# Kernel optimization log

Hardware: AMD Instinct MI355X
Metric: run time of the kernel (lower is better)

Reference implementation:

```python
import jax, jax.numpy as jnp
import numpy as np

HID = 2048
HEADS = 16
HD = HID // HEADS  # 128


def setup_inputs() -> dict:
    key = jax.random.key(0)
    ks = jax.random.split(key, 9)
    s = 0.02
    return {
        "hidden_state": jax.random.normal(ks[0], (2, 2048, HID), dtype=jnp.float32),
        "Wq": jax.random.normal(ks[1], (HID, HID), dtype=jnp.float32) * s,
        "bq": jnp.zeros((HID,), dtype=jnp.float32),
        "Wk": jax.random.normal(ks[2], (HID, HD), dtype=jnp.float32) * s,
        "bk": jnp.zeros((HD,), dtype=jnp.float32),
        "Wv": jax.random.normal(ks[3], (HID, HD), dtype=jnp.float32) * s,
        "bv": jnp.zeros((HD,), dtype=jnp.float32),
        "Wo": jax.random.normal(ks[4], (HID, HID), dtype=jnp.float32) * s,
        "bo": jnp.zeros((HID,), dtype=jnp.float32),
    }


def reference(hidden_state, Wq, bq, Wk, bk, Wv, bv, Wo, bo):
    bs, seq, _ = hidden_state.shape
    # Q: [b, s, H, hd] -> per-head; K,V: single shared head [b, s, hd]
    q = (hidden_state @ Wq + bq).reshape(bs, seq, HEADS, HD)
    k = hidden_state @ Wk + bk  # [b, s, hd]
    v = hidden_state @ Wv + bv  # [b, s, hd]
    scale = 1.0 / jnp.sqrt(jnp.float32(HD))
    # scores: [b, h, s_q, s_k] against shared K head
    scores = jnp.einsum("bqhd,bkd->bhqk", q, k) * scale
    attn = jax.nn.softmax(scores, axis=-1)
    out = jnp.einsum("bhqk,bkd->bqhd", attn, v)  # [b, s, h, hd]
    out = out.reshape(bs, seq, HID)
    return out @ Wo + bo
```

## Files before the change

### kernel.cpp

```cpp
#include <hip/hip_runtime.h>
#include <math.h>

#define HIDN 2048
#define NHEADS 16
#define HDIM 128
#define SEQ 2048
#define NB 2

typedef __bf16 bf16x8 __attribute__((ext_vector_type(8)));
typedef float f32x4 __attribute__((ext_vector_type(4)));

__device__ __forceinline__ unsigned short f32_to_bf16(float f) {
  unsigned int u = __float_as_uint(f);
  u += 0x7FFFu + ((u >> 16) & 1u);
  return (unsigned short)(u >> 16);
}

__device__ __forceinline__ unsigned pack_bf16x2(float a, float b) {
  return (unsigned)f32_to_bf16(a) | ((unsigned)f32_to_bf16(b) << 16);
}

__device__ __forceinline__ void gload_lds16(const void* g, void* l) {
  __builtin_amdgcn_global_load_lds(
      (__attribute__((address_space(1))) void*)(g),
      (__attribute__((address_space(3))) void*)(l), 16, 0, 0);
}

__global__ __launch_bounds__(256) void cast_f32_bf16(
    const float* __restrict__ in, unsigned short* __restrict__ out, int n4) {
  int i = blockIdx.x * blockDim.x + threadIdx.x;
  if (i >= n4) return;
  float4 v = ((const float4*)in)[i];
  ushort4 o;
  o.x = f32_to_bf16(v.x); o.y = f32_to_bf16(v.y);
  o.z = f32_to_bf16(v.z); o.w = f32_to_bf16(v.w);
  ((ushort4*)out)[i] = o;
}

__global__ __launch_bounds__(256) void wtrans_big(
    const float* __restrict__ wq, unsigned short* __restrict__ dq,
    const float* __restrict__ wo, unsigned short* __restrict__ do_) {
  __shared__ float tile[32][33];
  const float* src = blockIdx.z ? wo : wq;
  unsigned short* dst = blockIdx.z ? do_ : dq;
  int c0 = blockIdx.x * 32, r0 = blockIdx.y * 32;
  int tx = threadIdx.x & 31, ty = threadIdx.x >> 5;
#pragma unroll
  for (int i = 0; i < 32; i += 8)
    tile[ty + i][tx] = src[(size_t)(r0 + ty + i) * 2048 + c0 + tx];
  __syncthreads();
#pragma unroll
  for (int i = 0; i < 32; i += 8)
    dst[(size_t)(c0 + ty + i) * 2048 + r0 + tx] = f32_to_bf16(tile[tx][ty + i]);
}

__global__ __launch_bounds__(256) void wtrans_small(
    const float* __restrict__ wk, const float* __restrict__ wv,
    unsigned short* __restrict__ dk, unsigned short* __restrict__ dv,
    const float* __restrict__ bq, const float* __restrict__ bk,
    const float* __restrict__ bv, float* __restrict__ biasout) {
  __shared__ float tile[32][33];
  const float* src = blockIdx.z ? wv : wk;
  unsigned short* dst = blockIdx.z ? dv : dk;
  int c0 = blockIdx.x * 32, r0 = blockIdx.y * 32;
  int tx = threadIdx.x & 31, ty = threadIdx.x >> 5;
#pragma unroll
  for (int i = 0; i < 32; i += 8)
    tile[ty + i][tx] = src[(size_t)(r0 + ty + i) * 128 + c0 + tx];
  __syncthreads();
#pragma unroll
  for (int i = 0; i < 32; i += 8)
    dst[(size_t)(c0 + ty + i) * 2048 + r0 + tx] = f32_to_bf16(tile[tx][ty + i]);
  if (blockIdx.z == 0) {
    int lb = blockIdx.y * 4 + blockIdx.x;
    if (lb < 9) {
      int i = lb * 256 + threadIdx.x;
      if (i < 2304)
        biasout[i] = (i < 2048) ? bq[i] : ((i < 2176) ? bk[i - 2048] : bv[i - 2176]);
    }
  }
}

__global__ __launch_bounds__(256) void vtrans(
    const unsigned short* __restrict__ qkv, unsigned short* __restrict__ vt) {
  __shared__ unsigned short tile[32][33];
  const unsigned short* src = qkv + (size_t)blockIdx.z * SEQ * 2304 + 2176;
  unsigned short* dst = vt + (size_t)blockIdx.z * 128 * SEQ;
  int c0 = blockIdx.x * 32, r0 = blockIdx.y * 32;
  int tx = threadIdx.x & 31, ty = threadIdx.x >> 5;
#pragma unroll
  for (int i = 0; i < 32; i += 8)
    tile[ty + i][tx] = src[(size_t)(r0 + ty + i) * 2304 + c0 + tx];
  __syncthreads();
  const int s = r0 + tx;
  const int col = (s & ~63) | (((s >> 5) & 1) * 32 + ((s >> 2) & 3) * 8 +
                               ((s >> 4) & 1) * 4 + (s & 3));
#pragma unroll
  for (int i = 0; i < 32; i += 8)
    dst[(size_t)(c0 + ty + i) * SEQ + col] = tile[tx][ty + i];
}

template <int BN>
__global__ __launch_bounds__(256) void gemm_bt(
    const unsigned short* __restrict__ A,
    const unsigned short* __restrict__ BT,
    const float* __restrict__ bias,
    void* __restrict__ C, int K, int ldc, int outBf16) {
  constexpr int NT = BN / 32;
  __shared__ unsigned short As[128 * 64];
  __shared__ unsigned short Bs[BN * 64];
  const int tid = threadIdx.x;
  const int lane = tid & 63;
  const int wave = tid >> 6;
  const int wr = wave >> 1, wc = wave & 1;
  const int ml = lane & 15, quad = lane >> 4;
  const long bm = (long)blockIdx.x * 128;
  const long bn = (long)blockIdx.y * BN;

  const f32x4 zero4 = {0.f, 0.f, 0.f, 0.f};
  f32x4 acc[4][NT];
#pragma unroll
  for (int mt = 0; mt < 4; ++mt)
#pragma unroll
    for (int nt = 0; nt < NT; ++nt) acc[mt][nt] = zero4;

  const int srow = lane >> 3;
  const int scol = ((lane & 7) ^ srow) * 8;

  for (int k0 = 0; k0 < K; k0 += 64) {
    __syncthreads();
#pragma unroll
    for (int r = 0; r < 4; ++r) {
      const int rowb = r * 32 + wave * 8;
      gload_lds16(A + (bm + rowb + srow) * (long)K + k0 + scol, &As[rowb * 64]);
    }
#pragma unroll
    for (int r = 0; r < NT; ++r) {
      const int rowb = r * 32 + wave * 8;
      gload_lds16(BT + (bn + rowb + srow) * (long)K + k0 + scol, &Bs[rowb * 64]);
    }
    __syncthreads();
#pragma unroll
    for (int kk = 0; kk < 64; kk += 32) {
      const int g0 = (kk >> 3) + quad;
      bf16x8 af[4], bf[NT];
#pragma unroll
      for (int mt = 0; mt < 4; ++mt)
        af[mt] = *(const bf16x8*)&As[(wr * 64 + mt * 16 + ml) * 64 +
                                     ((g0 ^ (ml & 7)) << 3)];
#pragma unroll
      for (int nt = 0; nt < NT; ++nt)
        bf[nt] = *(const bf16x8*)&Bs[(wc * (BN / 2) + nt * 16 + ml) * 64 +
                                     ((g0 ^ (ml & 7)) << 3)];
#pragma unroll
      for (int mt = 0; mt < 4; ++mt)
#pragma unroll
        for (int nt = 0; nt < NT; ++nt)
          acc[mt][nt] = __builtin_amdgcn_mfma_f32_16x16x32_bf16(
              af[mt], bf[nt], acc[mt][nt], 0, 0, 0);
    }
  }

#pragma unroll
  for (int mt = 0; mt < 4; ++mt) {
#pragma unroll
    for (int nt = 0; nt < NT; ++nt) {
      const long col = bn + wc * (BN / 2) + nt * 16 + ml;
      const float bval = bias ? bias[col] : 0.f;
#pragma unroll
      for (int r = 0; r < 4; ++r) {
        const long row = bm + wr * 64 + mt * 16 + quad * 4 + r;
        const float v = acc[mt][nt][r] + bval;
        if (outBf16)
          ((unsigned short*)C)[row * ldc + col] = f32_to_bf16(v);
        else
          ((float*)C)[row * ldc + col] = v;
      }
    }
  }
}

__global__ __launch_bounds__(256, 2) void mqa_attn(
    const unsigned short* __restrict__ qkv,
    const unsigned short* __restrict__ vt,
    unsigned short* __restrict__ outp) {
  __shared__ unsigned short Ks[2][64 * 128];
  __shared__ unsigned short VTs[2][128 * 64];

  const int lane = threadIdx.x & 63;
  const int wave = threadIdx.x >> 6;
  const int ml = lane & 15, quad = lane >> 4;
  const int h = blockIdx.y, b = blockIdx.z;
  const long q0 = (long)blockIdx.x * 128;
  const long base = (long)b * SEQ;

  bf16x8 aq[2][4];
#pragma unroll
  for (int n = 0; n < 2; ++n) {
    const unsigned short* qrow =
        qkv + (base + q0 + wave * 32 + n * 16 + ml) * 2304 + h * 128;
#pragma unroll
    for (int ks = 0; ks < 4; ++ks)
      aq[n][ks] = *(const bf16x8*)(qrow + ks * 32 + quad * 8);
  }

  const f32x4 zero4 = {0.f, 0.f, 0.f, 0.f};
  f32x4 o[8][2];
#pragma unroll
  for (int mt2 = 0; mt2 < 8; ++mt2)
#pragma unroll
    for (int n = 0; n < 2; ++n) o[mt2][n] = zero4;
  float l[2] = {0.f, 0.f};
  const float c2 = 0.08838834764831845f * 1.4426950408889634f;

  const int srowK = lane >> 4;
  const int scolK = ((lane & 15) ^ (wave * 4 + srowK)) * 8;
  const int srowV = lane >> 3;
  const int scolV = ((lane & 7) ^ srowV) * 8;
  const unsigned short* kp = qkv + (base + srowK) * 2304 + 2048 + scolK;
  const unsigned short* vp = vt + ((long)b * 128 + srowV) * SEQ + scolV;

  auto stage = [&](int buf, int ktn) {
    const unsigned short* kpp = kp + (long)ktn * (64 * 2304);
    const unsigned short* vpp = vp + ktn * 64;
#pragma unroll
    for (int r = 0; r < 4; ++r) {
      const int rowb = r * 16 + wave * 4;
      gload_lds16(kpp + (long)rowb * 2304, &Ks[buf][rowb * 128]);
    }
#pragma unroll
    for (int r = 0; r < 4; ++r) {
      const int rowb = r * 32 + wave * 8;
      gload_lds16(vpp + (long)rowb * SEQ, &VTs[buf][rowb * 64]);
    }
  };

  stage(0, 0);

  for (int kt = 0; kt < SEQ / 64; ++kt) {
    const int cur = kt & 1;
    __syncthreads();
    if (kt < SEQ / 64 - 1) stage(cur ^ 1, kt + 1);

    f32x4 s[4][2];
#pragma unroll
    for (int mt = 0; mt < 4; ++mt)
#pragma unroll
      for (int n = 0; n < 2; ++n) s[mt][n] = zero4;
#pragma unroll
    for (int ks = 0; ks < 4; ++ks) {
#pragma unroll
      for (int mt = 0; mt < 4; ++mt) {
        bf16x8 ak = *(const bf16x8*)&Ks[cur][(mt * 16 + ml) * 128 +
                                            (((ks * 4 + quad) ^ ml) << 3)];
#pragma unroll
        for (int n = 0; n < 2; ++n)
          s[mt][n] = __builtin_amdgcn_mfma_f32_16x16x32_bf16(
              ak, aq[n][ks], s[mt][n], 0, 0, 0);
      }
    }

    unsigned pk[2][4][2];
#pragma unroll
    for (int mt = 0; mt < 4; ++mt)
#pragma unroll
      for (int n = 0; n < 2; ++n) {
        const float p0 = exp2f(s[mt][n][0] * c2);
        const float p1 = exp2f(s[mt][n][1] * c2);
        const float p2 = exp2f(s[mt][n][2] * c2);
        const float p3 = exp2f(s[mt][n][3] * c2);
        l[n] += (p0 + p1) + (p2 + p3);
        pk[n][mt][0] = pack_bf16x2(p0, p1);
        pk[n][mt][1] = pack_bf16x2(p2, p3);
      }

#pragma unroll
    for (int ks2 = 0; ks2 < 2; ++ks2) {
      bf16x8 bp[2];
#pragma unroll
      for (int n = 0; n < 2; ++n) {
        union { unsigned u[4]; bf16x8 v; } cv;
        cv.u[0] = pk[n][2 * ks2][0];
        cv.u[1] = pk[n][2 * ks2][1];
        cv.u[2] = pk[n][2 * ks2 + 1][0];
        cv.u[3] = pk[n][2 * ks2 + 1][1];
        bp[n] = cv.v;
      }
#pragma unroll
      for (int mt2 = 0; mt2 < 8; ++mt2) {
        bf16x8 av = *(const bf16x8*)&VTs[cur][(mt2 * 16 + ml) * 64 +
                                             (((ks2 * 4 + quad) ^ (ml & 7)) << 3)];
#pragma unroll
        for (int n = 0; n < 2; ++n)
          o[mt2][n] = __builtin_amdgcn_mfma_f32_16x16x32_bf16(
              av, bp[n], o[mt2][n], 0, 0, 0);
      }
    }
  }

  float inv[2];
#pragma unroll
  for (int n = 0; n < 2; ++n) {
    float rs = l[n];
    rs += __shfl_xor(rs, 16);
    rs += __shfl_xor(rs, 32);
    inv[n] = 1.f / rs;
  }
#pragma unroll
  for (int n = 0; n < 2; ++n) {
    const long row = base + q0 + wave * 32 + n * 16 + ml;
#pragma unroll
    for (int mt2 = 0; mt2 < 8; ++mt2) {
      uint2 w;
      w.x = pack_bf16x2(o[mt2][n][0] * inv[n], o[mt2][n][1] * inv[n]);
      w.y = pack_bf16x2(o[mt2][n][2] * inv[n], o[mt2][n][3] * inv[n]);
      *(uint2*)&outp[row * HIDN + h * HDIM + mt2 * 16 + quad * 4] = w;
    }
  }
}

extern "C" void kernel_launch(void* const* d_in, const int* in_sizes, int n_in,
                              void* d_out, int out_size, void* d_ws, size_t ws_size,
                              hipStream_t stream) {
  const float* hidden = (const float*)d_in[0];
  const float* Wq = (const float*)d_in[1];
  const float* bq = (const float*)d_in[2];
  const float* Wk = (const float*)d_in[3];
  const float* bk = (const float*)d_in[4];
  const float* Wv = (const float*)d_in[5];
  const float* bv = (const float*)d_in[6];
  const float* Wo = (const float*)d_in[7];
  const float* bo = (const float*)d_in[8];
  float* out = (float*)d_out;

  char* ws = (char*)d_ws;
  const size_t MB = 1u << 20;
  unsigned short* hb    = (unsigned short*)(ws);
  unsigned short* attn  = hb;
  unsigned short* wqkvT = (unsigned short*)(ws + 16 * MB);
  unsigned short* woT   = (unsigned short*)(ws + 25 * MB);
  unsigned short* qkv   = (unsigned short*)(ws + 33 * MB);
  unsigned short* vt    = (unsigned short*)(ws + 51 * MB);
  float* biasqkv        = (float*)(ws + 52 * MB);

  cast_f32_bf16<<<8192, 256, 0, stream>>>(hidden, hb, (NB * SEQ * HIDN) / 4);
  wtrans_big<<<dim3(64, 64, 2), 256, 0, stream>>>(Wq, wqkvT, Wo, woT);
  wtrans_small<<<dim3(4, 64, 2), 256, 0, stream>>>(
      Wk, Wv, wqkvT + (size_t)2048 * 2048, wqkvT + (size_t)2176 * 2048,
      bq, bk, bv, biasqkv);

  gemm_bt<96><<<dim3(32, 24), 256, 0, stream>>>(hb, wqkvT, biasqkv, qkv, 2048, 2304, 1);

  vtrans<<<dim3(4, 64, 2), 256, 0, stream>>>(qkv, vt);

  mqa_attn<<<dim3(SEQ / 128, NHEADS, NB), 256, 0, stream>>>(qkv, vt, attn);

  gemm_bt<128><<<dim3(32, 16), 256, 0, stream>>>(attn, woT, bo, out, 2048, 2048, 0);
}
```

Measured before the change: 317.9 us.

## Fold softmax scale into Wq, use MFMA row-sum, read V directly from global

Folds the softmax scale and log2e factor into the bf16 conversion of Wq and bq, so the attention kernel can call the raw hardware exp2 with no multiply. Replaces the per-lane row-sum accumulation and final shuffles with an extra MFMA against a ones vector. Converts P to bf16 by truncation through a byte permute instead of round-to-nearest. Drops the V LDS staging and loads V fragments straight from global memory into registers each tile, which frees LDS but adds register pressure and global-load latency inside the loop.

Result: slower. 356.8 us (+12.3%).

```diff
diff --git a/kernel.cpp b/kernel.cpp
--- a/kernel.cpp
+++ b/kernel.cpp
@@ -7,6 +7,8 @@
 #define SEQ 2048
 #define NB 2
 
+#define C2 0.12751744154f
+
 typedef __bf16 bf16x8 __attribute__((ext_vector_type(8)));
 typedef float f32x4 __attribute__((ext_vector_type(4)));
 
@@ -18,6 +20,10 @@
 
 __device__ __forceinline__ unsigned pack_bf16x2(float a, float b) {
   return (unsigned)f32_to_bf16(a) | ((unsigned)f32_to_bf16(b) << 16);
+}
+
+__device__ __forceinline__ unsigned pack_bf16x2_trunc(float a, float b) {
+  return __builtin_amdgcn_perm(__float_as_uint(b), __float_as_uint(a), 0x07060302u);
 }
 
 __device__ __forceinline__ void gload_lds16(const void* g, void* l) {
@@ -43,6 +49,7 @@
   __shared__ float tile[32][33];
   const float* src = blockIdx.z ? wo : wq;
   unsigned short* dst = blockIdx.z ? do_ : dq;
+  const float m = blockIdx.z ? 1.0f : C2;
   int c0 = blockIdx.x * 32, r0 = blockIdx.y * 32;
   int tx = threadIdx.x & 31, ty = threadIdx.x >> 5;
 #pragma unroll
@@ -51,7 +58,7 @@
   __syncthreads();
 #pragma unroll
   for (int i = 0; i < 32; i += 8)
-    dst[(size_t)(c0 + ty + i) * 2048 + r0 + tx] = f32_to_bf16(tile[tx][ty + i]);
+    dst[(size_t)(c0 + ty + i) * 2048 + r0 + tx] = f32_to_bf16(tile[tx][ty + i] * m);
 }
 
 __global__ __launch_bounds__(256) void wtrans_small(
@@ -76,7 +83,8 @@
     if (lb < 9) {
       int i = lb * 256 + threadIdx.x;
       if (i < 2304)
-        biasout[i] = (i < 2048) ? bq[i] : ((i < 2176) ? bk[i - 2048] : bv[i - 2176]);
+        biasout[i] = (i < 2048) ? bq[i] * C2
+                                : ((i < 2176) ? bk[i - 2048] : bv[i - 2176]);
     }
   }
 }
@@ -185,7 +193,6 @@
     const unsigned short* __restrict__ vt,
     unsigned short* __restrict__ outp) {
   __shared__ unsigned short Ks[2][64 * 128];
-  __shared__ unsigned short VTs[2][128 * 64];
 
   const int lane = threadIdx.x & 63;
   const int wave = threadIdx.x >> 6;
@@ -210,37 +217,47 @@
   for (int mt2 = 0; mt2 < 8; ++mt2)
 #pragma unroll
     for (int n = 0; n < 2; ++n) o[mt2][n] = zero4;
-  float l[2] = {0.f, 0.f};
-  const float c2 = 0.08838834764831845f * 1.4426950408889634f;
+  f32x4 o9[2] = {zero4, zero4};
+
+  bf16x8 ones_af;
+  {
+    union { unsigned u[4]; bf16x8 v; } cv;
+    const unsigned w = (ml == 0) ? 0x3F803F80u : 0u;
+    cv.u[0] = w; cv.u[1] = w; cv.u[2] = w; cv.u[3] = w;
+    ones_af = cv.v;
+  }
 
   const int srowK = lane >> 4;
   const int scolK = ((lane & 15) ^ (wave * 4 + srowK)) * 8;
-  const int srowV = lane >> 3;
-  const int scolV = ((lane & 7) ^ srowV) * 8;
   const unsigned short* kp = qkv + (base + srowK) * 2304 + 2048 + scolK;
-  const unsigned short* vp = vt + ((long)b * 128 + srowV) * SEQ + scolV;
-
-  auto stage = [&](int buf, int ktn) {
+
+  const unsigned short* vb[8];
+#pragma unroll
+  for (int mt2 = 0; mt2 < 8; ++mt2)
+    vb[mt2] = vt + ((long)b * 128 + mt2 * 16 + ml) * SEQ + quad * 8;
+
+  auto stageK = [&](int buf, int ktn) {
     const unsigned short* kpp = kp + (long)ktn * (64 * 2304);
-    const unsigned short* vpp = vp + ktn * 64;
 #pragma unroll
     for (int r = 0; r < 4; ++r) {
       const int rowb = r * 16 + wave * 4;
       gload_lds16(kpp + (long)rowb * 2304, &Ks[buf][rowb * 128]);
     }
-#pragma unroll
-    for (int r = 0; r < 4; ++r) {
-      const int rowb = r * 32 + wave * 8;
-      gload_lds16(vpp + (long)rowb * SEQ, &VTs[buf][rowb * 64]);
-    }
   };
 
-  stage(0, 0);
+  stageK(0, 0);
 
   for (int kt = 0; kt < SEQ / 64; ++kt) {
     const int cur = kt & 1;
     __syncthreads();
-    if (kt < SEQ / 64 - 1) stage(cur ^ 1, kt + 1);
+    if (kt < SEQ / 64 - 1) stageK(cur ^ 1, kt + 1);
+
+    bf16x8 av[8][2];
+#pragma unroll
+    for (int mt2 = 0; mt2 < 8; ++mt2)
+#pragma unroll
+      for (int ks2 = 0; ks2 < 2; ++ks2)
+        av[mt2][ks2] = *(const bf16x8*)(vb[mt2] + kt * 64 + ks2 * 32);
 
     f32x4 s[4][2];
 #pragma unroll
@@ -265,13 +282,12 @@
     for (int mt = 0; mt < 4; ++mt)
 #pragma unroll
       for (int n = 0; n < 2; ++n) {
-        const float p0 = exp2f(s[mt][n][0] * c2);
-        const float p1 = exp2f(s[mt][n][1] * c2);
-        const float p2 = exp2f(s[mt][n][2] * c2);
-        const float p3 = exp2f(s[mt][n][3] * c2);
-        l[n] += (p0 + p1) + (p2 + p3);
-        pk[n][mt][0] = pack_bf16x2(p0, p1);
-        pk[n][mt][1] = pack_bf16x2(p2, p3);
+        const float p0 = __builtin_amdgcn_exp2f(s[mt][n][0]);
+        const float p1 = __builtin_amdgcn_exp2f(s[mt][n][1]);
+        const float p2 = __builtin_amdgcn_exp2f(s[mt][n][2]);
+        const float p3 = __builtin_amdgcn_exp2f(s[mt][n][3]);
+        pk[n][mt][0] = pack_bf16x2_trunc(p0, p1);
+        pk[n][mt][1] = pack_bf16x2_trunc(p2, p3);
       }
 
 #pragma unroll
@@ -287,25 +303,24 @@
         bp[n] = cv.v;
       }
 #pragma unroll
+      for (int n = 0; n < 2; ++n)
+        o9[n] = __builtin_amdgcn_mfma_f32_16x16x32_bf16(
+            ones_af, bp[n], o9[n], 0, 0, 0);
+#pragma unroll
       for (int mt2 = 0; mt2 < 8; ++mt2) {
-        bf16x8 av = *(const bf16x8*)&VTs[cur][(mt2 * 16 + ml) * 64 +
-                                             (((ks2 * 4 + quad) ^ (ml & 7)) << 3)];
 #pragma unroll
         for (int n = 0; n < 2; ++n)
           o[mt2][n] = __builtin_amdgcn_mfma_f32_16x16x32_bf16(
-              av, bp[n], o[mt2][n], 0, 0, 0);
+              av[mt2][ks2], bp[n], o[mt2][n], 0, 0, 0);
       }
     }
   }
 
   float inv[2];
 #pragma unroll
-  for (int n = 0; n < 2; ++n) {
-    float rs = l[n];
-    rs += __shfl_xor(rs, 16);
-    rs += __shfl_xor(rs, 32);
-    inv[n] = 1.f / rs;
-  }
+  for (int n = 0; n < 2; ++n)
+    inv[n] = 1.f / __shfl(o9[n][0], ml);
+
 #pragma unroll
   for (int n = 0; n < 2; ++n) {
     const long row = base + q0 + wave * 32 + n * 16 + ml;
```
